# Kernel tuning notes

Hardware: AMD Instinct MI355X
Metric: run time of the kernel (lower is better)

Reference implementation:

```python
import jax, jax.numpy as jnp
import numpy as np

Na, Ns, Nb, Ne, MAXLEN, D = 16, 64, 100, 12, 20, 512
EPS = 1e-5
DELTA = 0.2
VIS_LAM = 1.0


def _make_boxes(key, shape):
    u = jax.random.uniform(key, shape + (4,), dtype=jnp.float32)
    xy = u[..., :2] * 0.7
    wh = u[..., 2:] * 0.3 + 0.01
    return jnp.concatenate([xy, xy + wh], axis=-1)  # valid xyxy boxes


def setup_inputs() -> dict:
    key = jax.random.key(0)
    k1, k2, k3, k4, k5 = jax.random.split(key, 5)
    return {
        "vis_feats": jax.random.normal(k1, (Na * Ns * Nb, D), dtype=jnp.float32),
        "word_feats": jax.random.normal(k2, (Na * Ne, D), dtype=jnp.float32),
        "boxes": _make_boxes(k3, (Na, Ns, Nb)),
        "detect_boxes": _make_boxes(k4, (Na, MAXLEN)),
        "entities_length": jax.random.randint(k5, (Na,), 0, Ne, dtype=jnp.int32),
    }


def _iou(a, b):
    # a, b: broadcastable (..., 4) xyxy. Same math as DVSA.IOU, vectorized.
    iw = jnp.minimum(a[..., 2], b[..., 2]) - jnp.maximum(a[..., 0], b[..., 0])
    ih = jnp.minimum(a[..., 3], b[..., 3]) - jnp.maximum(a[..., 1], b[..., 1])
    pos = (iw > 0) & (ih > 0)
    inter = jnp.where(pos, iw * ih, 0.0)
    a1 = (a[..., 2] - a[..., 0]) * (a[..., 3] - a[..., 1])
    a2 = (b[..., 2] - b[..., 0]) * (b[..., 3] - b[..., 1])
    denom = a1 + a2 - inter
    return jnp.where(pos, inter / jnp.where(denom > 0, denom, 1.0), 0.0)


def reference(vis_feats, word_feats, boxes, detect_boxes, entities_length):
    ar = jnp.arange(Na)
    div_vec = jnp.maximum(entities_length, 1).astype(vis_feats.dtype)          # zero2one
    word_mask = jnp.arange(Ne)[None, :] >= entities_length[:, None]            # (Na, Ne) True = padded entity

    # Ragged-masked similarity: (Na*Ns*Nb, Na*Ne)
    S_ = vis_feats @ word_feats.T
    S_ = jnp.where(word_mask.reshape(-1)[None, :], 0.0, S_)

    # Pairwise box IoU table (Na, Ns, Nb, MAXLEN) -- vectorized quadruple loop
    d_ti_n = _iou(boxes[:, :, :, None, :], detect_boxes[:, None, None, :, :])

    # --- visual consistency loss (train phase) ---
    S5 = S_.reshape(Na, Ns, Nb, Na, Ne)
    S_vis = S5[ar, :, :, ar, :]                                                # (Na, Ns, Nb, Ne) diagonal video<->caption
    sim_scr = jnp.max(S_vis, axis=2)                                           # (Na, Ns, Ne)
    maxind = jnp.argmax(S_vis, axis=2)                                         # best box per (video, seg, entity)
    flat_ind = (ar[:, None, None] * Ns + jnp.arange(Ns)[None, :, None]) * Nb + maxind
    mn = sim_scr.min(axis=1, keepdims=True)
    mx = sim_scr.max(axis=1, keepdims=True)
    sim_scr = jax.lax.stop_gradient((sim_scr - mn) / (mx - mn + EPS))[..., None]
    flat_ind = jax.lax.stop_gradient(flat_ind)

    v = vis_feats[flat_ind.reshape(-1)].reshape(Na, Ns, Ne, D)
    v = v / (jnp.linalg.norm(v, axis=3, keepdims=True) + EPS) * sim_scr
    v1 = v.transpose(0, 2, 1, 3).reshape(Na * Ne, Ns, D)
    gram = 1.0 - jnp.einsum('bsd,btd->bst', v1, v1).reshape(Na, Ne, Ns, Ns)
    eye = jnp.eye(Ns, dtype=bool)
    vis_mask = word_mask[:, :, None, None] | eye[None, None, :, :]
    gram = jnp.where(vis_mask, 0.0, gram)
    dem = jnp.maximum(jnp.count_nonzero(gram), 1).astype(gram.dtype)
    vis_loss = gram.sum() / dem

    # --- frame / margin score ---
    S = S_.reshape(Na * Ns, Nb, Na * Ne).max(axis=1).reshape(Na, Ns, Na * Ne)
    mn = S.min(axis=1, keepdims=True)
    mx = S.max(axis=1, keepdims=True)
    S = S * (S - mn) / (mx - mn + EPS)
    Sf = S.reshape(Na, Ns, Na, Ne).sum(axis=-1) / div_vec[None, None, :]        # (Na, Ns, Na)
    Sf_diag = Sf[ar, :, ar]                                                     # (Na, Ns)
    term1 = jax.nn.relu(Sf - Sf_diag.T[None, :, :] + DELTA).mean(axis=0).T      # (Na, Ns)
    term2 = jax.nn.relu(Sf - Sf_diag[:, :, None] + DELTA).mean(axis=2)          # (Na, Ns)
    frame_score = term1 + term2
    margin_loss = (frame_score.mean() + VIS_LAM * vis_loss) * 10.0

    S_sim = S_.reshape(Na * Ns, Nb, Na * Ne)
    D_sim = S_sim.max(axis=1)
    D_ind = S_sim.argmax(axis=1)
    return (D_ind, D_sim, margin_loss, d_ti_n)
```

## Files before the change

kernel.cpp:

```cpp
#include <hip/hip_runtime.h>
#include <math.h>

#define NA 16
#define NS 64
#define NB 100
#define NE 12
#define ML 20
#define DD 512
#define NC (NA*NE)
#define NR (NA*NS)
#define EPSF 1e-5f
#define DELTA_F 0.2f
#define IOU_TOTAL (NA*NS*NB*ML)
#define IOU_BLOCKS ((IOU_TOTAL + 255)/256)

__device__ inline void wave_minmax64(float v, float& mn, float& mx){
  mn = v; mx = v;
  #pragma unroll
  for (int off = 32; off > 0; off >>= 1){
    mn = fminf(mn, __shfl_xor(mn, off));
    mx = fmaxf(mx, __shfl_xor(mx, off));
  }
}

__device__ inline float block_sum256(float v, float* sred){
  int t = threadIdx.x;
  #pragma unroll
  for (int off = 32; off > 0; off >>= 1) v += __shfl_xor(v, off);
  if ((t & 63) == 0) sred[t >> 6] = v;
  __syncthreads();
  float tot = sred[0] + sred[1] + sred[2] + sred[3];
  __syncthreads();
  return tot;
}

template<int JC>
__device__ __forceinline__ void gemm_pass(
    const float* __restrict__ abase, const float* __restrict__ word,
    const int* __restrict__ scols, float* __restrict__ As, float* __restrict__ Bs,
    int t, int tc, int tb)
{
  float acc[7][JC];
  #pragma unroll
  for (int j = 0; j < 7; ++j)
    #pragma unroll
    for (int jc = 0; jc < JC; ++jc) acc[j][jc] = 0.f;

  for (int k0 = 0; k0 < DD; k0 += 32){
    for (int i = t; i < NB * 8; i += 256){
      int b = i >> 3, q = i & 7;
      const float4 v = *(const float4*)(abase + (size_t)b * DD + k0 + q * 4);
      float* d = &As[b * 33 + q * 4];
      d[0] = v.x; d[1] = v.y; d[2] = v.z; d[3] = v.w;
    }
    for (int i = t; i < JC * 16 * 8; i += 256){
      int c = i >> 3, q = i & 7;
      const float4 v = *(const float4*)(word + (size_t)scols[c] * DD + k0 + q * 4);
      float* d = &Bs[c * 33 + q * 4];
      d[0] = v.x; d[1] = v.y; d[2] = v.z; d[3] = v.w;
    }
    __syncthreads();
    #pragma unroll 4
    for (int kk = 0; kk < 32; ++kk){
      float breg[JC], areg[7];
      #pragma unroll
      for (int jc = 0; jc < JC; ++jc) breg[jc] = Bs[(jc * 16 + tc) * 33 + kk];
      #pragma unroll
      for (int j = 0; j < 7; ++j){
        int b = tb * 7 + j; b = (b < NB) ? b : (NB - 1);
        areg[j] = As[b * 33 + kk];
      }
      #pragma unroll
      for (int j = 0; j < 7; ++j)
        #pragma unroll
        for (int jc = 0; jc < JC; ++jc)
          acc[j][jc] = fmaf(areg[j], breg[jc], acc[j][jc]);
    }
    __syncthreads();
  }
  #pragma unroll
  for (int jc = 0; jc < JC; ++jc){
    int ci = jc * 16 + tc;
    float best = -3.4e38f; int bi = 0;
    #pragma unroll
    for (int j = 0; j < 7; ++j){
      int b = tb * 7 + j;
      if (b < NB){ float v = acc[j][jc]; if (v > best){ best = v; bi = b; } }
    }
    As[ci * 16 + tb] = best;
    Bs[ci * 16 + tb] = (float)bi;
  }
}

__device__ __forceinline__ void gemm_epilogue(
    const float* __restrict__ As, const float* __restrict__ Bs,
    const int* __restrict__ scols, int base, int ncols, int kcnt,
    float* __restrict__ dsim, float* __restrict__ dind, int r, int t)
{
  __syncthreads();
  if (t < ncols){
    int gi = base + t;
    if (gi < kcnt){
      float best = -3.4e38f; int bi = 0;
      #pragma unroll
      for (int g = 0; g < 16; ++g){
        float v = As[t * 16 + g];
        if (v > best){ best = v; bi = (int)Bs[t * 16 + g]; }
      }
      int c = scols[gi];
      dsim[r * NC + c] = best;
      dind[r * NC + c] = (float)bi;
    }
  }
  __syncthreads();
}

__global__ __launch_bounds__(256) void k_main(
    const float* __restrict__ vis, const float* __restrict__ word,
    const int* __restrict__ elen, const float* __restrict__ boxes,
    const float* __restrict__ det,
    float* __restrict__ dind, float* __restrict__ dsim, float* __restrict__ dtin)
{
  const int t = threadIdx.x;

  if (blockIdx.x >= NR){
    int idx = (int)(blockIdx.x - NR) * 256 + t;
    if (idx < IOU_TOTAL){
      int m = idx % ML; int t2 = idx / ML; int b = t2 % NB; int t3 = t2 / NB;
      const float4 A = *(const float4*)(boxes + (size_t)(t3 * NB + b) * 4);
      int a = t3 / NS;
      const float4 B = *(const float4*)(det + (size_t)(a * ML + m) * 4);
      float iw = fminf(A.z, B.z) - fmaxf(A.x, B.x);
      float ih = fminf(A.w, B.w) - fmaxf(A.y, B.y);
      bool pos = (iw > 0.f) && (ih > 0.f);
      float inter = pos ? iw * ih : 0.f;
      float a1 = (A.z - A.x) * (A.w - A.y);
      float a2 = (B.z - B.x) * (B.w - B.y);
      float den = a1 + a2 - inter;
      dtin[idx] = pos ? inter / (den > 0.f ? den : 1.f) : 0.f;
    }
    return;
  }

  __shared__ float As[NB * 33];
  __shared__ float Bs[128 * 33];
  __shared__ int   scols[NC];
  __shared__ int   s_el[NA];
  __shared__ int   s_cnt;
  const int r  = blockIdx.x;
  const int tc = t & 15;
  const int tb = t >> 4;

  if (t < NA){ int L = elen[t]; L = L < 0 ? 0 : (L > NE ? NE : L); s_el[t] = L; }
  if (t < NC){ dsim[r * NC + t] = 0.f; dind[r * NC + t] = 0.f; }
  __syncthreads();
  if (t < NC){
    int aw = t / NE, e = t - aw * NE;
    int base = 0;
    #pragma unroll
    for (int i = 0; i < NA; ++i) base += (i < aw) ? s_el[i] : 0;
    if (e < s_el[aw]) scols[base + e] = t;
  }
  if (t == 0){
    int n = 0;
    #pragma unroll
    for (int i = 0; i < NA; ++i) n += s_el[i];
    s_cnt = n;
  }
  __syncthreads();
  const int kcnt = s_cnt;
  if (t < NC && t >= kcnt) scols[t] = (kcnt > 0) ? scols[kcnt - 1] : 0;
  __syncthreads();

  const int jcnt = (kcnt + 15) >> 4;
  if (jcnt == 0) return;
  const float* abase = vis + (size_t)r * NB * DD;

  const int jc1 = (jcnt > 8) ? 8 : jcnt;
  switch (jc1){
    case 1: gemm_pass<1>(abase, word, scols, As, Bs, t, tc, tb); break;
    case 2: gemm_pass<2>(abase, word, scols, As, Bs, t, tc, tb); break;
    case 3: gemm_pass<3>(abase, word, scols, As, Bs, t, tc, tb); break;
    case 4: gemm_pass<4>(abase, word, scols, As, Bs, t, tc, tb); break;
    case 5: gemm_pass<5>(abase, word, scols, As, Bs, t, tc, tb); break;
    case 6: gemm_pass<6>(abase, word, scols, As, Bs, t, tc, tb); break;
    case 7: gemm_pass<7>(abase, word, scols, As, Bs, t, tc, tb); break;
    default: gemm_pass<8>(abase, word, scols, As, Bs, t, tc, tb); break;
  }
  gemm_epilogue(As, Bs, scols, 0, jc1 * 16, kcnt, dsim, dind, r, t);

  if (jcnt > 8){
    const int jc2 = jcnt - 8;
    switch (jc2){
      case 1: gemm_pass<1>(abase, word, scols + 128, As, Bs, t, tc, tb); break;
      case 2: gemm_pass<2>(abase, word, scols + 128, As, Bs, t, tc, tb); break;
      case 3: gemm_pass<3>(abase, word, scols + 128, As, Bs, t, tc, tb); break;
      default: gemm_pass<4>(abase, word, scols + 128, As, Bs, t, tc, tb); break;
    }
    gemm_epilogue(As, Bs, scols, 128, jc2 * 16, kcnt, dsim, dind, r, t);
  }
}

__global__ void k_sfsim(const float* __restrict__ dsim, const int* __restrict__ elen,
                        float* __restrict__ sf, float* __restrict__ simn,
                        float* __restrict__ accums)
{
  int a = blockIdx.x, aw = blockIdx.y, s = threadIdx.x;
  if (a == 0 && aw == 0 && s == 0){ accums[0] = 0.f; accums[1] = 0.f; }
  const bool diag = (aw == a);
  float accv = 0.f;
  for (int e = 0; e < NE; ++e){
    int c = aw * NE + e;
    float v = dsim[(a * NS + s) * NC + c];
    float mn, mx; wave_minmax64(v, mn, mx);
    float nv = (v - mn) / (mx - mn + EPSF);
    accv += v * nv;
    if (diag) simn[(a * NS + s) * NE + e] = nv;
  }
  float dv = fmaxf((float)elen[aw], 1.f);
  sf[(a * NS + s) * NA + aw] = accv / dv;
}

__global__ __launch_bounds__(256) void k_gram(
    const float* __restrict__ vis, const float* __restrict__ dind,
    const float* __restrict__ simn, const int* __restrict__ elen,
    float* __restrict__ accums)
{
  const int a = blockIdx.x, e = blockIdx.y;
  if (e >= elen[a]) return;
  __shared__ int   s_mi[NS];
  __shared__ float s_inv[NS];
  __shared__ float s_nw2[NS];
  __shared__ float sred[4];
  const int t = threadIdx.x, lane = t & 63, w = t >> 6;

  if (t < NS) s_mi[t] = (int)dind[(size_t)(a * NS + t) * NC + (a * NE + e)];
  __syncthreads();

  for (int s = w; s < NS; s += 4){
    const float* row = vis + (size_t)((a * NS + s) * NB + s_mi[s]) * DD;
    float4 v0 = *(const float4*)(row + lane * 8);
    float4 v1 = *(const float4*)(row + lane * 8 + 4);
    float ss = v0.x*v0.x + v0.y*v0.y + v0.z*v0.z + v0.w*v0.w
             + v1.x*v1.x + v1.y*v1.y + v1.z*v1.z + v1.w*v1.w;
    #pragma unroll
    for (int off = 32; off > 0; off >>= 1) ss += __shfl_xor(ss, off);
    if (lane == 0){
      float sn = simn[(size_t)(a * NS + s) * NE + e];
      float d = sqrtf(ss) + EPSF;
      s_inv[s] = sn / d;
      s_nw2[s] = sn * sn * ss / (d * d);
    }
  }
  __syncthreads();

  float W0 = 0.f, W1 = 0.f;
  #pragma unroll 8
  for (int s = 0; s < NS; ++s){
    const float* row = vis + (size_t)((a * NS + s) * NB + s_mi[s]) * DD;
    float inv = s_inv[s];
    W0 = fmaf(row[t],       inv, W0);
    W1 = fmaf(row[t + 256], inv, W1);
  }
  float w2  = block_sum256(W0 * W0 + W1 * W1, sred);
  float nw2 = block_sum256((t < NS) ? s_nw2[t] : 0.f, sred);
  if (t == 0){
    float part = (float)(NS * (NS - 1)) - w2 + nw2;
    atomicAdd(&accums[0], part);
    atomicAdd(&accums[1], (float)(NS * (NS - 1)));
  }
}

__global__ __launch_bounds__(256) void k_final(
    const float* __restrict__ sf, const float* __restrict__ accums, float* __restrict__ out)
{
  __shared__ float sred[4];
  int t = threadIdx.x;
  float sum = 0.f;
  for (int i = t; i < NA * NS * NA; i += 256){
    int b = i & (NA - 1);
    int s = (i >> 4) & (NS - 1);
    int a = i >> 10;
    float v  = sf[i];
    float d1 = sf[(b * NS + s) * NA + b];
    float d2 = sf[(a * NS + s) * NA + a];
    sum += fmaxf(v - d1 + DELTA_F, 0.f) + fmaxf(v - d2 + DELTA_F, 0.f);
  }
  float tot = block_sum256(sum, sred);
  if (t == 0){
    float frame = tot / (float)(NA * NA * NS);
    float cnt = accums[1];
    float vis_loss = accums[0] / fmaxf(cnt, 1.f);
    out[0] = (frame + vis_loss) * 10.f;
  }
}

extern "C" void kernel_launch(void* const* d_in, const int* in_sizes, int n_in,
                              void* d_out, int out_size, void* d_ws, size_t ws_size,
                              hipStream_t stream)
{
  const float* vis   = (const float*)d_in[0];
  const float* word  = (const float*)d_in[1];
  const float* boxes = (const float*)d_in[2];
  const float* det   = (const float*)d_in[3];
  const int*   elen  = (const int*)d_in[4];

  float* out   = (float*)d_out;
  float* dind  = out;
  float* dsim  = out + NR * NC;
  float* mloss = out + 2 * NR * NC;
  float* dtin  = mloss + 1;

  float* ws     = (float*)d_ws;
  float* sf     = ws;
  float* simn   = ws + NA * NS * NA;
  float* accums = simn + NA * NS * NE;

  k_main<<<NR + IOU_BLOCKS, 256, 0, stream>>>(vis, word, elen, boxes, det, dind, dsim, dtin);
  k_sfsim<<<dim3(NA, NA), 64, 0, stream>>>(dsim, elen, sf, simn, accums);
  k_gram<<<dim3(NA, NE), 256, 0, stream>>>(vis, dind, simn, elen, accums);
  k_final<<<1, 256, 0, stream>>>(sf, accums, mloss);
}
```

Baseline: 521.1 us.

## Fuse post-GEMM kernels into one last-block-reduce kernel and vectorize LDS reads

Merges the sf/simn, gram and final kernels into a single kernel. Each gram block recomputes its diagonal normalized similarity itself, and the last block to finish, detected with an atomic counter, performs the final margin reduction. This removes two kernel launches and the simn round trip through memory. Separately, the GEMM shared-memory pitch changes from 33 to 34 so the inner loop can read float2 pairs from LDS, halving the number of LDS read instructions at the cost of possible bank conflicts.

```diff
diff --git a/kernel.cpp b/kernel.cpp
--- a/kernel.cpp
+++ b/kernel.cpp
@@ -13,6 +13,8 @@
 #define DELTA_F 0.2f
 #define IOU_TOTAL (NA*NS*NB*ML)
 #define IOU_BLOCKS ((IOU_TOTAL + 255)/256)
+#define PIT 34
+#define MID_BLOCKS (NA*(NE+1))
 
 __device__ inline void wave_minmax64(float v, float& mn, float& mx){
   mn = v; mx = v;
@@ -50,31 +52,38 @@
     for (int i = t; i < NB * 8; i += 256){
       int b = i >> 3, q = i & 7;
       const float4 v = *(const float4*)(abase + (size_t)b * DD + k0 + q * 4);
-      float* d = &As[b * 33 + q * 4];
-      d[0] = v.x; d[1] = v.y; d[2] = v.z; d[3] = v.w;
+      float* d = &As[b * PIT + q * 4];
+      *(float2*)d       = make_float2(v.x, v.y);
+      *(float2*)(d + 2) = make_float2(v.z, v.w);
     }
     for (int i = t; i < JC * 16 * 8; i += 256){
       int c = i >> 3, q = i & 7;
       const float4 v = *(const float4*)(word + (size_t)scols[c] * DD + k0 + q * 4);
-      float* d = &Bs[c * 33 + q * 4];
-      d[0] = v.x; d[1] = v.y; d[2] = v.z; d[3] = v.w;
+      float* d = &Bs[c * PIT + q * 4];
+      *(float2*)d       = make_float2(v.x, v.y);
+      *(float2*)(d + 2) = make_float2(v.z, v.w);
     }
     __syncthreads();
     #pragma unroll 4
-    for (int kk = 0; kk < 32; ++kk){
-      float breg[JC], areg[7];
+    for (int kk = 0; kk < 32; kk += 2){
+      float2 breg[JC], areg[7];
       #pragma unroll
-      for (int jc = 0; jc < JC; ++jc) breg[jc] = Bs[(jc * 16 + tc) * 33 + kk];
+      for (int jc = 0; jc < JC; ++jc)
+        breg[jc] = *(const float2*)&Bs[(jc * 16 + tc) * PIT + kk];
       #pragma unroll
       for (int j = 0; j < 7; ++j){
         int b = tb * 7 + j; b = (b < NB) ? b : (NB - 1);
-        areg[j] = As[b * 33 + kk];
+        areg[j] = *(const float2*)&As[b * PIT + kk];
       }
       #pragma unroll
       for (int j = 0; j < 7; ++j)
         #pragma unroll
-        for (int jc = 0; jc < JC; ++jc)
-          acc[j][jc] = fmaf(areg[j], breg[jc], acc[j][jc]);
+        for (int jc = 0; jc < JC; ++jc){
+          float s0 = acc[j][jc];
+          s0 = fmaf(areg[j].x, breg[jc].x, s0);
+          s0 = fmaf(areg[j].y, breg[jc].y, s0);
+          acc[j][jc] = s0;
+        }
     }
     __syncthreads();
   }
@@ -119,7 +128,8 @@
     const float* __restrict__ vis, const float* __restrict__ word,
     const int* __restrict__ elen, const float* __restrict__ boxes,
     const float* __restrict__ det,
-    float* __restrict__ dind, float* __restrict__ dsim, float* __restrict__ dtin)
+    float* __restrict__ dind, float* __restrict__ dsim, float* __restrict__ dtin,
+    float* __restrict__ accums, unsigned int* __restrict__ done)
 {
   const int t = threadIdx.x;
 
@@ -142,14 +152,16 @@
     return;
   }
 
-  __shared__ float As[NB * 33];
-  __shared__ float Bs[128 * 33];
+  __shared__ float As[NB * PIT];
+  __shared__ float Bs[128 * PIT];
   __shared__ int   scols[NC];
   __shared__ int   s_el[NA];
   __shared__ int   s_cnt;
   const int r  = blockIdx.x;
   const int tc = t & 15;
   const int tb = t >> 4;
+
+  if (r == 0 && t == 0){ accums[0] = 0.f; accums[1] = 0.f; done[0] = 0u; }
 
   if (t < NA){ int L = elen[t]; L = L < 0 ? 0 : (L > NE ? NE : L); s_el[t] = L; }
   if (t < NC){ dsim[r * NC + t] = 0.f; dind[r * NC + t] = 0.f; }
@@ -201,97 +213,105 @@
   }
 }
 
-__global__ void k_sfsim(const float* __restrict__ dsim, const int* __restrict__ elen,
-                        float* __restrict__ sf, float* __restrict__ simn,
-                        float* __restrict__ accums)
-{
-  int a = blockIdx.x, aw = blockIdx.y, s = threadIdx.x;
-  if (a == 0 && aw == 0 && s == 0){ accums[0] = 0.f; accums[1] = 0.f; }
-  const bool diag = (aw == a);
-  float accv = 0.f;
-  for (int e = 0; e < NE; ++e){
-    int c = aw * NE + e;
-    float v = dsim[(a * NS + s) * NC + c];
-    float mn, mx; wave_minmax64(v, mn, mx);
-    float nv = (v - mn) / (mx - mn + EPSF);
-    accv += v * nv;
-    if (diag) simn[(a * NS + s) * NE + e] = nv;
-  }
-  float dv = fmaxf((float)elen[aw], 1.f);
-  sf[(a * NS + s) * NA + aw] = accv / dv;
-}
-
-__global__ __launch_bounds__(256) void k_gram(
+__global__ __launch_bounds__(256) void k_mid(
     const float* __restrict__ vis, const float* __restrict__ dind,
-    const float* __restrict__ simn, const int* __restrict__ elen,
-    float* __restrict__ accums)
-{
-  const int a = blockIdx.x, e = blockIdx.y;
-  if (e >= elen[a]) return;
+    const float* __restrict__ dsim, const int* __restrict__ elen,
+    float* __restrict__ sf, float* __restrict__ accums,
+    unsigned int* __restrict__ done, float* __restrict__ out)
+{
+  const int a = blockIdx.x, y = blockIdx.y;
+  const int t = threadIdx.x, lane = t & 63, w = t >> 6;
+  __shared__ float sred[4];
   __shared__ int   s_mi[NS];
   __shared__ float s_inv[NS];
   __shared__ float s_nw2[NS];
-  __shared__ float sred[4];
-  const int t = threadIdx.x, lane = t & 63, w = t >> 6;
-
-  if (t < NS) s_mi[t] = (int)dind[(size_t)(a * NS + t) * NC + (a * NE + e)];
-  __syncthreads();
-
-  for (int s = w; s < NS; s += 4){
-    const float* row = vis + (size_t)((a * NS + s) * NB + s_mi[s]) * DD;
-    float4 v0 = *(const float4*)(row + lane * 8);
-    float4 v1 = *(const float4*)(row + lane * 8 + 4);
-    float ss = v0.x*v0.x + v0.y*v0.y + v0.z*v0.z + v0.w*v0.w
-             + v1.x*v1.x + v1.y*v1.y + v1.z*v1.z + v1.w*v1.w;
-    #pragma unroll
-    for (int off = 32; off > 0; off >>= 1) ss += __shfl_xor(ss, off);
-    if (lane == 0){
-      float sn = simn[(size_t)(a * NS + s) * NE + e];
-      float d = sqrtf(ss) + EPSF;
-      s_inv[s] = sn / d;
-      s_nw2[s] = sn * sn * ss / (d * d);
-    }
-  }
-  __syncthreads();
-
-  float W0 = 0.f, W1 = 0.f;
-  #pragma unroll 8
-  for (int s = 0; s < NS; ++s){
-    const float* row = vis + (size_t)((a * NS + s) * NB + s_mi[s]) * DD;
-    float inv = s_inv[s];
-    W0 = fmaf(row[t],       inv, W0);
-    W1 = fmaf(row[t + 256], inv, W1);
-  }
-  float w2  = block_sum256(W0 * W0 + W1 * W1, sred);
-  float nw2 = block_sum256((t < NS) ? s_nw2[t] : 0.f, sred);
+  __shared__ float s_sn[NS];
+  __shared__ int   s_last;
+
+  if (y == NE){
+    for (int aw = w; aw < NA; aw += 4){
+      float accv = 0.f;
+      for (int e = 0; e < NE; ++e){
+        int c = aw * NE + e;
+        float v = dsim[(a * NS + lane) * NC + c];
+        float mn, mx; wave_minmax64(v, mn, mx);
+        accv += v * (v - mn) / (mx - mn + EPSF);
+      }
+      float dv = fmaxf((float)elen[aw], 1.f);
+      sf[(a * NS + lane) * NA + aw] = accv / dv;
+    }
+  } else {
+    const int e = y;
+    if (e < elen[a]){
+      if (w == 0){
+        float v = dsim[(a * NS + lane) * NC + (a * NE + e)];
+        float mn, mx; wave_minmax64(v, mn, mx);
+        s_sn[lane] = (v - mn) / (mx - mn + EPSF);
+      }
+      if (t < NS) s_mi[t] = (int)dind[(size_t)(a * NS + t) * NC + (a * NE + e)];
+      __syncthreads();
+
+      for (int s = w; s < NS; s += 4){
+        const float* row = vis + (size_t)((a * NS + s) * NB + s_mi[s]) * DD;
+        float4 v0 = *(const float4*)(row + lane * 8);
+        float4 v1 = *(const float4*)(row + lane * 8 + 4);
+        float ss = v0.x*v0.x + v0.y*v0.y + v0.z*v0.z + v0.w*v0.w
+                 + v1.x*v1.x + v1.y*v1.y + v1.z*v1.z + v1.w*v1.w;
+        #pragma unroll
+        for (int off = 32; off > 0; off >>= 1) ss += __shfl_xor(ss, off);
+        if (lane == 0){
+          float sn = s_sn[s];
+          float d = sqrtf(ss) + EPSF;
+          s_inv[s] = sn / d;
+          s_nw2[s] = sn * sn * ss / (d * d);
+        }
+      }
+      __syncthreads();
+
+      float W0 = 0.f, W1 = 0.f;
+      #pragma unroll 8
+      for (int s = 0; s < NS; ++s){
+        const float* row = vis + (size_t)((a * NS + s) * NB + s_mi[s]) * DD;
+        float inv = s_inv[s];
+        W0 = fmaf(row[t],       inv, W0);
+        W1 = fmaf(row[t + 256], inv, W1);
+      }
+      float w2  = block_sum256(W0 * W0 + W1 * W1, sred);
+      float nw2 = block_sum256((t < NS) ? s_nw2[t] : 0.f, sred);
+      if (t == 0){
+        float part = (float)(NS * (NS - 1)) - w2 + nw2;
+        atomicAdd(&accums[0], part);
+        atomicAdd(&accums[1], (float)(NS * (NS - 1)));
+      }
+    }
+  }
+
+  __syncthreads();
   if (t == 0){
-    float part = (float)(NS * (NS - 1)) - w2 + nw2;
-    atomicAdd(&accums[0], part);
-    atomicAdd(&accums[1], (float)(NS * (NS - 1)));
-  }
-}
-
-__global__ __launch_bounds__(256) void k_final(
-    const float* __restrict__ sf, const float* __restrict__ accums, float* __restrict__ out)
-{
-  __shared__ float sred[4];
-  int t = threadIdx.x;
-  float sum = 0.f;
-  for (int i = t; i < NA * NS * NA; i += 256){
-    int b = i & (NA - 1);
-    int s = (i >> 4) & (NS - 1);
-    int a = i >> 10;
-    float v  = sf[i];
-    float d1 = sf[(b * NS + s) * NA + b];
-    float d2 = sf[(a * NS + s) * NA + a];
-    sum += fmaxf(v - d1 + DELTA_F, 0.f) + fmaxf(v - d2 + DELTA_F, 0.f);
-  }
-  float tot = block_sum256(sum, sred);
-  if (t == 0){
-    float frame = tot / (float)(NA * NA * NS);
-    float cnt = accums[1];
-    float vis_loss = accums[0] / fmaxf(cnt, 1.f);
-    out[0] = (frame + vis_loss) * 10.f;
+    __threadfence();
+    unsigned int old = atomicAdd(done, 1u);
+    s_last = (old == (unsigned int)(MID_BLOCKS - 1)) ? 1 : 0;
+  }
+  __syncthreads();
+  if (s_last){
+    __threadfence();
+    float sum = 0.f;
+    for (int i = t; i < NA * NS * NA; i += 256){
+      int b = i & (NA - 1);
+      int a2 = i >> 10;
+      float v  = sf[i];
+      int s2 = (i >> 4) & (NS - 1);
+      float d1 = sf[(b * NS + s2) * NA + b];
+      float d2 = sf[(a2 * NS + s2) * NA + a2];
+      sum += fmaxf(v - d1 + DELTA_F, 0.f) + fmaxf(v - d2 + DELTA_F, 0.f);
+    }
+    float tot = block_sum256(sum, sred);
+    if (t == 0){
+      float frame = tot / (float)(NA * NA * NS);
+      float cnt = accums[1];
+      float vis_loss = accums[0] / fmaxf(cnt, 1.f);
+      out[0] = (frame + vis_loss) * 10.f;
+    }
   }
 }
 
@@ -313,11 +333,11 @@
 
   float* ws     = (float*)d_ws;
   float* sf     = ws;
-  float* simn   = ws + NA * NS * NA;
-  float* accums = simn + NA * NS * NE;
-
-  k_main<<<NR + IOU_BLOCKS, 256, 0, stream>>>(vis, word, elen, boxes, det, dind, dsim, dtin);
-  k_sfsim<<<dim3(NA, NA), 64, 0, stream>>>(dsim, elen, sf, simn, accums);
-  k_gram<<<dim3(NA, NE), 256, 0, stream>>>(vis, dind, simn, elen, accums);
-  k_final<<<1, 256, 0, stream>>>(sf, accums, mloss);
-}
+  float* accums = ws + NA * NS * NA;
+  unsigned int* done = (unsigned int*)(accums + 2);
+
+  k_main<<<NR + IOU_BLOCKS, 256, 0, stream>>>(vis, word, elen, boxes, det,
+                                              dind, dsim, dtin, accums, done);
+  k_mid<<<dim3(NA, NE + 1), 256, 0, stream>>>(vis, dind, dsim, elen,
+                                              sf, accums, done, mloss);
+}
```

Result: faster. 505.7 us (-3.0%).
